# Kernel tuning notes

Hardware: AMD Instinct MI355X
Metric: run time of the kernel (lower is better)

## Reference

```python
import jax, jax.numpy as jnp
import numpy as np

N_NODES = 50000
N_EDGES = 800000
FEAT_DIM = 64


def setup_inputs() -> dict:
    key = jax.random.key(0)
    k1, k2, k3 = jax.random.split(key, 3)
    x = jax.random.normal(k1, (N_NODES, FEAT_DIM), dtype=jnp.float32)
    beta = jnp.ones((1,), dtype=jnp.float32)
    # CSR-equivalent edge list: sorted destination rows + random source columns
    row_index = jnp.sort(jax.random.randint(k2, (N_EDGES,), 0, N_NODES, dtype=jnp.int32))
    col_index = jax.random.randint(k3, (N_EDGES,), 0, N_NODES, dtype=jnp.int32)
    return {"x": x, "beta": beta, "row_index": row_index, "col_index": col_index}


def reference(x, beta, row_index, col_index):
    """AGNN layer: SDDMM edge attention (beta * cosine similarity) over the
    sparse graph, per-row softmax, then sparse neighbor aggregation.
    Equivalent math to mygraph.SDDMM + mygraph.agnn_udf (select_id == 5).
    x: [N, D]; row_index/col_index: [E] edge endpoints (row = destination).
    """
    N = x.shape[0]
    eps = 1e-8
    # L2-normalize node features for cosine similarity
    xn = x * jax.lax.rsqrt(jnp.sum(x * x, axis=-1, keepdims=True) + eps)  # [N, D]
    # SDDMM: attention only on existing edges
    att = beta[0] * jnp.sum(xn[row_index] * xn[col_index], axis=-1)  # [E]
    # Numerically stable segment softmax over each destination row
    m = jax.ops.segment_max(att, row_index, num_segments=N)  # [N]
    m = jnp.where(jnp.isfinite(m), m, 0.0)  # empty rows -> -inf guard
    e = jnp.exp(att - m[row_index])  # [E]
    denom = jax.ops.segment_sum(e, row_index, num_segments=N)  # [N]
    alpha = e / jnp.maximum(denom[row_index], 1e-16)  # [E]
    # Sparse aggregation: out_i = sum_j alpha_ij * x_j
    out = jax.ops.segment_sum(alpha[:, None] * x[col_index], row_index, num_segments=N)
    return out
```

## Files before the change

### kernel.cpp

```cpp
#include <hip/hip_runtime.h>
#include <hip/hip_bf16.h>

#define FEAT 64

__global__ void prep_kernel(const float* __restrict__ x,
                            float* __restrict__ rn,
                            const int* __restrict__ row,
                            int* __restrict__ row_ptr,
                            int N, int E, int normBlocks) {
    if ((int)blockIdx.x < normBlocks) {
        int wid  = blockIdx.x * (blockDim.x >> 6) + (threadIdx.x >> 6);
        int lane = threadIdx.x & 63;
        int g    = lane >> 3;
        int sub  = lane & 7;
        int r    = wid * 8 + g;
        if (r >= N) return;
        const char* xB = (const char*)x;
        uint roff = ((uint)r << 8) + ((uint)sub << 4);
        float4 xa = *reinterpret_cast<const float4*>(xB + roff);
        float4 xb = *reinterpret_cast<const float4*>(xB + roff + 128);
        float q = xa.x*xa.x + xa.y*xa.y + xa.z*xa.z + xa.w*xa.w
                + xb.x*xb.x + xb.y*xb.y + xb.z*xb.z + xb.w*xb.w;
        q += __shfl_xor(q, 1);
        q += __shfl_xor(q, 2);
        q += __shfl_xor(q, 4);
        if (sub == 0) rn[r] = rsqrtf(q + 1e-8f);
    } else {
        int e = (blockIdx.x - normBlocks) * blockDim.x + threadIdx.x;
        if (e >= E) return;
        int curr = row[e];
        if (e == 0) {
            for (int r = 0; r <= curr; ++r) row_ptr[r] = 0;
        } else {
            int prev = row[e - 1];
            for (int r = prev + 1; r <= curr; ++r) row_ptr[r] = e;
        }
        if (e == E - 1) {
            for (int r = curr + 1; r <= N; ++r) row_ptr[r] = E;
        }
    }
}

__global__ void fused_kernel(const float* __restrict__ x,
                             const float* __restrict__ rn,
                             const float* __restrict__ beta,
                             const int* __restrict__ row_ptr,
                             const int* __restrict__ col,
                             float* __restrict__ out, int N) {
    int wid  = blockIdx.x * (blockDim.x >> 6) + (threadIdx.x >> 6);
    int lane = threadIdx.x & 63;
    int slot = lane >> 4;
    int h    = (lane >> 3) & 1;
    int sub  = lane & 7;
    int r    = wid * 4 + slot;
    bool rv  = (r < N);

    int start = 0, deg = 0;
    if (rv) {
        start = row_ptr[r];
        deg   = row_ptr[r + 1] - start;
    }

    const char* xB   = (const char*)x;
    uint        subo = (uint)sub << 4;

    int   colsA = 0, colsB = 0;
    float rnsA  = 0.f, rnsB = 0.f;
    if (sub < deg)     { colsA = col[start + sub];     rnsA = rn[colsA]; }
    if (8 + sub < deg) { colsB = col[start + 8 + sub]; rnsB = rn[colsB]; }

    float4 xa = make_float4(0.f, 0.f, 0.f, 0.f);
    float4 xb = make_float4(0.f, 0.f, 0.f, 0.f);
    if (rv) {
        uint roff = ((uint)r << 8) + subo;
        xa = *reinterpret_cast<const float4*>(xB + roff);
        xb = *reinterpret_cast<const float4*>(xB + roff + 128);
        float brn = beta[0] * rn[r];
        xa.x *= brn; xa.y *= brn; xa.z *= brn; xa.w *= brn;
        xb.x *= brn; xb.y *= brn; xb.z *= brn; xb.w *= brn;
    }

    float  s = 0.f;
    float4 aa = make_float4(0.f, 0.f, 0.f, 0.f);
    float4 ab = make_float4(0.f, 0.f, 0.f, 0.f);

    for (int base = 0; base < deg; base += 4) {
        if (base && (base & 7) == 0) {
            colsA = colsB;  rnsA = rnsB;
            if (base + 8 + sub < deg) {
                colsB = col[start + base + 8 + sub];
                rnsB  = rn[colsB];
            }
        }
        int  k0 = base + 2 * h;
        int  kk = (base & 7) + 2 * h;
        bool v0 = k0 < deg;
        bool v1 = k0 + 1 < deg;

        int   c0  = __shfl(colsA, kk, 8);
        float rn0 = __shfl(rnsA,  kk, 8);
        int   c1  = __shfl(colsA, kk + 1, 8);
        float rn1 = __shfl(rnsA,  kk + 1, 8);

        float4 va0 = make_float4(0.f, 0.f, 0.f, 0.f);
        float4 vb0 = make_float4(0.f, 0.f, 0.f, 0.f);
        float4 va1 = make_float4(0.f, 0.f, 0.f, 0.f);
        float4 vb1 = make_float4(0.f, 0.f, 0.f, 0.f);
        if (v0) {
            uint o0 = ((uint)c0 << 8) + subo;
            va0 = *reinterpret_cast<const float4*>(xB + o0);
            vb0 = *reinterpret_cast<const float4*>(xB + o0 + 128);
        }
        if (v1) {
            uint o1 = ((uint)c1 << 8) + subo;
            va1 = *reinterpret_cast<const float4*>(xB + o1);
            vb1 = *reinterpret_cast<const float4*>(xB + o1 + 128);
        }

        float d0 = xa.x*va0.x + xa.y*va0.y + xa.z*va0.z + xa.w*va0.w
                 + xb.x*vb0.x + xb.y*vb0.y + xb.z*vb0.z + xb.w*vb0.w;
        float d1 = xa.x*va1.x + xa.y*va1.y + xa.z*va1.z + xa.w*va1.w
                 + xb.x*vb1.x + xb.y*vb1.y + xb.z*vb1.z + xb.w*vb1.w;
        d0 += __shfl_xor(d0, 1);  d1 += __shfl_xor(d1, 1);
        d0 += __shfl_xor(d0, 2);  d1 += __shfl_xor(d1, 2);
        d0 += __shfl_xor(d0, 4);  d1 += __shfl_xor(d1, 4);

        float e0 = v0 ? __expf(d0 * rn0) : 0.f;
        float e1 = v1 ? __expf(d1 * rn1) : 0.f;
        s += e0 + e1;

        aa.x += e0 * va0.x + e1 * va1.x;  aa.y += e0 * va0.y + e1 * va1.y;
        aa.z += e0 * va0.z + e1 * va1.z;  aa.w += e0 * va0.w + e1 * va1.w;
        ab.x += e0 * vb0.x + e1 * vb1.x;  ab.y += e0 * vb0.y + e1 * vb1.y;
        ab.z += e0 * vb0.z + e1 * vb1.z;  ab.w += e0 * vb0.w + e1 * vb1.w;
    }

    s    += __shfl_xor(s, 8);
    aa.x += __shfl_xor(aa.x, 8);  aa.y += __shfl_xor(aa.y, 8);
    aa.z += __shfl_xor(aa.z, 8);  aa.w += __shfl_xor(aa.w, 8);
    ab.x += __shfl_xor(ab.x, 8);  ab.y += __shfl_xor(ab.y, 8);
    ab.z += __shfl_xor(ab.z, 8);  ab.w += __shfl_xor(ab.w, 8);

    float inv = 1.0f / fmaxf(s, 1e-16f);
    if (rv) {
        float4 o = h ? ab : aa;
        uint roff = ((uint)r << 8) + subo + ((uint)h << 7);
        *reinterpret_cast<float4*>((char*)out + roff) =
            make_float4(o.x * inv, o.y * inv, o.z * inv, o.w * inv);
    }
}

extern "C" void kernel_launch(void* const* d_in, const int* in_sizes, int n_in,
                              void* d_out, int out_size, void* d_ws, size_t ws_size,
                              hipStream_t stream) {
    const float* x    = (const float*)d_in[0];
    const float* beta = (const float*)d_in[1];
    const int*   row  = (const int*)d_in[2];
    const int*   col  = (const int*)d_in[3];
    float*       out  = (float*)d_out;

    const int N = in_sizes[0] / FEAT;
    const int E = in_sizes[2];

    float* rn      = (float*)d_ws;
    int*   row_ptr = (int*)(rn + ((N + 63) & ~63));

    {
        int normBlocks = (N + 31) / 32;
        int edgeBlocks = (E + 255) / 256;
        prep_kernel<<<normBlocks + edgeBlocks, 256, 0, stream>>>(
            x, rn, row, row_ptr, N, E, normBlocks);
    }
    {
        int waves = (N + 3) / 4;
        int grid  = (waves + 3) / 4;
        fused_kernel<<<grid, 256, 0, stream>>>(x, rn, beta, row_ptr, col, out, N);
    }
}
```

Before: 40.03 us.

## Gather neighbor features from a bf16 copy with software-pipelined prefetch

The prep kernel now also writes a bf16-packed copy of x (128 bytes per row) into the workspace. A new fused kernel gathers neighbor rows from that copy, which halves gather bytes. It processes 8 rows per wave with 4 edges per iteration and prefetches the next group's packed rows before computing the current one. Neighbor features used in both the attention dot product and the aggregation are rounded to bf16, which adds accuracy risk, and the path only runs when the workspace is large enough.

New measurement: 38.29 us. -4.3%, faster.

```diff
diff --git a/kernel.cpp b/kernel.cpp
--- a/kernel.cpp
+++ b/kernel.cpp
@@ -3,8 +3,27 @@
 
 #define FEAT 64
 
+__device__ inline uint packbf2(float lo, float hi) {
+    uint ul = __float_as_uint(lo), uh = __float_as_uint(hi);
+    ul += 0x7FFFu + ((ul >> 16) & 1u);
+    uh += 0x7FFFu + ((uh >> 16) & 1u);
+    return (ul >> 16) | (uh & 0xFFFF0000u);
+}
+
+__device__ inline void unpack8(uint4 q, float4& va, float4& vb) {
+    va.x = __uint_as_float(q.x << 16);
+    va.y = __uint_as_float(q.x & 0xFFFF0000u);
+    va.z = __uint_as_float(q.y << 16);
+    va.w = __uint_as_float(q.y & 0xFFFF0000u);
+    vb.x = __uint_as_float(q.z << 16);
+    vb.y = __uint_as_float(q.z & 0xFFFF0000u);
+    vb.z = __uint_as_float(q.w << 16);
+    vb.w = __uint_as_float(q.w & 0xFFFF0000u);
+}
+
 __global__ void prep_kernel(const float* __restrict__ x,
                             float* __restrict__ rn,
+                            uint4* __restrict__ xh,
                             const int* __restrict__ row,
                             int* __restrict__ row_ptr,
                             int N, int E, int normBlocks) {
@@ -25,6 +44,14 @@
         q += __shfl_xor(q, 2);
         q += __shfl_xor(q, 4);
         if (sub == 0) rn[r] = rsqrtf(q + 1e-8f);
+        if (xh) {
+            uint4 p;
+            p.x = packbf2(xa.x, xa.y);
+            p.y = packbf2(xa.z, xa.w);
+            p.z = packbf2(xb.x, xb.y);
+            p.w = packbf2(xb.z, xb.w);
+            xh[r * 8 + sub] = p;
+        }
     } else {
         int e = (blockIdx.x - normBlocks) * blockDim.x + threadIdx.x;
         if (e >= E) return;
@@ -38,6 +65,133 @@
         if (e == E - 1) {
             for (int r = curr + 1; r <= N; ++r) row_ptr[r] = E;
         }
+    }
+}
+
+__global__ void fused_bf16_kernel(const float* __restrict__ x,
+                                  const uint4* __restrict__ xh,
+                                  const float* __restrict__ rn,
+                                  const float* __restrict__ beta,
+                                  const int* __restrict__ row_ptr,
+                                  const int* __restrict__ col,
+                                  float* __restrict__ out, int N) {
+    int wid  = blockIdx.x * (blockDim.x >> 6) + (threadIdx.x >> 6);
+    int lane = threadIdx.x & 63;
+    int g    = lane >> 3;
+    int sub  = lane & 7;
+    int r    = wid * 8 + g;
+    bool rv  = (r < N);
+
+    int start = 0, deg = 0;
+    if (rv) {
+        start = row_ptr[r];
+        deg   = row_ptr[r + 1] - start;
+    }
+
+    int   colsA = 0, colsB = 0;
+    float rnsA  = 0.f, rnsB = 0.f;
+    if (sub < deg)     { colsA = col[start + sub];     rnsA = rn[colsA]; }
+    if (8 + sub < deg) { colsB = col[start + 8 + sub]; rnsB = rn[colsB]; }
+
+    float4 xa = make_float4(0.f, 0.f, 0.f, 0.f);
+    float4 xb = make_float4(0.f, 0.f, 0.f, 0.f);
+    if (rv) {
+        const char* xB = (const char*)x;
+        uint roff = ((uint)r << 8) + ((uint)sub << 4);
+        xa = *reinterpret_cast<const float4*>(xB + roff);
+        xb = *reinterpret_cast<const float4*>(xB + roff + 128);
+        float brn = beta[0] * rn[r];
+        xa.x *= brn; xa.y *= brn; xa.z *= brn; xa.w *= brn;
+        xb.x *= brn; xb.y *= brn; xb.z *= brn; xb.w *= brn;
+    }
+
+    float  s = 0.f;
+    float4 aa = make_float4(0.f, 0.f, 0.f, 0.f);
+    float4 ab = make_float4(0.f, 0.f, 0.f, 0.f);
+
+    uint4 z4 = make_uint4(0u, 0u, 0u, 0u);
+    uint4 q0 = z4, q1 = z4, q2 = z4, q3 = z4;
+    float rn0 = 0.f, rn1 = 0.f, rn2 = 0.f, rn3 = 0.f;
+
+    {
+        int   c0 = __shfl(colsA, 0, 8), c1 = __shfl(colsA, 1, 8);
+        int   c2 = __shfl(colsA, 2, 8), c3 = __shfl(colsA, 3, 8);
+        rn0 = __shfl(rnsA, 0, 8);  rn1 = __shfl(rnsA, 1, 8);
+        rn2 = __shfl(rnsA, 2, 8);  rn3 = __shfl(rnsA, 3, 8);
+        if (0 < deg) q0 = xh[c0 * 8 + sub];
+        if (1 < deg) q1 = xh[c1 * 8 + sub];
+        if (2 < deg) q2 = xh[c2 * 8 + sub];
+        if (3 < deg) q3 = xh[c3 * 8 + sub];
+    }
+
+    for (int base = 0; base < deg; base += 4) {
+        if (base && (base & 7) == 0) {
+            colsA = colsB;  rnsA = rnsB;
+            colsB = 0;      rnsB = 0.f;
+            if (base + 8 + sub < deg) {
+                colsB = col[start + base + 8 + sub];
+                rnsB  = rn[colsB];
+            }
+        }
+        int  nb  = base + 4;
+        int  nkk = nb & 7;
+        int   cS = (nkk == 4) ? colsA : colsB;
+        float rS = (nkk == 4) ? rnsA  : rnsB;
+        int   nc0 = __shfl(cS, nkk + 0, 8), nc1 = __shfl(cS, nkk + 1, 8);
+        int   nc2 = __shfl(cS, nkk + 2, 8), nc3 = __shfl(cS, nkk + 3, 8);
+        float nr0 = __shfl(rS, nkk + 0, 8), nr1 = __shfl(rS, nkk + 1, 8);
+        float nr2 = __shfl(rS, nkk + 2, 8), nr3 = __shfl(rS, nkk + 3, 8);
+        uint4 nq0 = z4, nq1 = z4, nq2 = z4, nq3 = z4;
+        if (nb + 0 < deg) nq0 = xh[nc0 * 8 + sub];
+        if (nb + 1 < deg) nq1 = xh[nc1 * 8 + sub];
+        if (nb + 2 < deg) nq2 = xh[nc2 * 8 + sub];
+        if (nb + 3 < deg) nq3 = xh[nc3 * 8 + sub];
+
+        float4 va0, vb0, va1, vb1, va2, vb2, va3, vb3;
+        unpack8(q0, va0, vb0);  unpack8(q1, va1, vb1);
+        unpack8(q2, va2, vb2);  unpack8(q3, va3, vb3);
+
+        float d0 = xa.x*va0.x + xa.y*va0.y + xa.z*va0.z + xa.w*va0.w
+                 + xb.x*vb0.x + xb.y*vb0.y + xb.z*vb0.z + xb.w*vb0.w;
+        float d1 = xa.x*va1.x + xa.y*va1.y + xa.z*va1.z + xa.w*va1.w
+                 + xb.x*vb1.x + xb.y*vb1.y + xb.z*vb1.z + xb.w*vb1.w;
+        float d2 = xa.x*va2.x + xa.y*va2.y + xa.z*va2.z + xa.w*va2.w
+                 + xb.x*vb2.x + xb.y*vb2.y + xb.z*vb2.z + xb.w*vb2.w;
+        float d3 = xa.x*va3.x + xa.y*va3.y + xa.z*va3.z + xa.w*va3.w
+                 + xb.x*vb3.x + xb.y*vb3.y + xb.z*vb3.z + xb.w*vb3.w;
+        d0 += __shfl_xor(d0, 1);  d1 += __shfl_xor(d1, 1);
+        d2 += __shfl_xor(d2, 1);  d3 += __shfl_xor(d3, 1);
+        d0 += __shfl_xor(d0, 2);  d1 += __shfl_xor(d1, 2);
+        d2 += __shfl_xor(d2, 2);  d3 += __shfl_xor(d3, 2);
+        d0 += __shfl_xor(d0, 4);  d1 += __shfl_xor(d1, 4);
+        d2 += __shfl_xor(d2, 4);  d3 += __shfl_xor(d3, 4);
+
+        float e0 = (base + 0 < deg) ? __expf(d0 * rn0) : 0.f;
+        float e1 = (base + 1 < deg) ? __expf(d1 * rn1) : 0.f;
+        float e2 = (base + 2 < deg) ? __expf(d2 * rn2) : 0.f;
+        float e3 = (base + 3 < deg) ? __expf(d3 * rn3) : 0.f;
+        s += (e0 + e1) + (e2 + e3);
+
+        aa.x += e0*va0.x + e1*va1.x + e2*va2.x + e3*va3.x;
+        aa.y += e0*va0.y + e1*va1.y + e2*va2.y + e3*va3.y;
+        aa.z += e0*va0.z + e1*va1.z + e2*va2.z + e3*va3.z;
+        aa.w += e0*va0.w + e1*va1.w + e2*va2.w + e3*va3.w;
+        ab.x += e0*vb0.x + e1*vb1.x + e2*vb2.x + e3*vb3.x;
+        ab.y += e0*vb0.y + e1*vb1.y + e2*vb2.y + e3*vb3.y;
+        ab.z += e0*vb0.z + e1*vb1.z + e2*vb2.z + e3*vb3.z;
+        ab.w += e0*vb0.w + e1*vb1.w + e2*vb2.w + e3*vb3.w;
+
+        q0 = nq0; q1 = nq1; q2 = nq2; q3 = nq3;
+        rn0 = nr0; rn1 = nr1; rn2 = nr2; rn3 = nr3;
+    }
+
+    float inv = 1.0f / fmaxf(s, 1e-16f);
+    if (rv) {
+        uint roff = ((uint)r << 8) + ((uint)sub << 4);
+        *reinterpret_cast<float4*>((char*)out + roff) =
+            make_float4(aa.x * inv, aa.y * inv, aa.z * inv, aa.w * inv);
+        *reinterpret_cast<float4*>((char*)out + roff + 128) =
+            make_float4(ab.x * inv, ab.y * inv, ab.z * inv, ab.w * inv);
     }
 }
 
@@ -98,9 +252,9 @@
         bool v1 = k0 + 1 < deg;
 
         int   c0  = __shfl(colsA, kk, 8);
-        float rn0 = __shfl(rnsA,  kk, 8);
+        float rw0 = __shfl(rnsA,  kk, 8);
         int   c1  = __shfl(colsA, kk + 1, 8);
-        float rn1 = __shfl(rnsA,  kk + 1, 8);
+        float rw1 = __shfl(rnsA,  kk + 1, 8);
 
         float4 va0 = make_float4(0.f, 0.f, 0.f, 0.f);
         float4 vb0 = make_float4(0.f, 0.f, 0.f, 0.f);
@@ -125,8 +279,8 @@
         d0 += __shfl_xor(d0, 2);  d1 += __shfl_xor(d1, 2);
         d0 += __shfl_xor(d0, 4);  d1 += __shfl_xor(d1, 4);
 
-        float e0 = v0 ? __expf(d0 * rn0) : 0.f;
-        float e1 = v1 ? __expf(d1 * rn1) : 0.f;
+        float e0 = v0 ? __expf(d0 * rw0) : 0.f;
+        float e1 = v1 ? __expf(d1 * rw1) : 0.f;
         s += e0 + e1;
 
         aa.x += e0 * va0.x + e1 * va1.x;  aa.y += e0 * va0.y + e1 * va1.y;
@@ -162,18 +316,30 @@
     const int N = in_sizes[0] / FEAT;
     const int E = in_sizes[2];
 
-    float* rn      = (float*)d_ws;
-    int*   row_ptr = (int*)(rn + ((N + 63) & ~63));
+    char*  ws      = (char*)d_ws;
+    size_t off_rp  = ((size_t)(N + 64) * 4 + 511) & ~(size_t)511;
+    size_t off_xh  = off_rp + (((size_t)(N + 1) * 4 + 511) & ~(size_t)511);
+    size_t need    = off_xh + (size_t)N * 128;
+
+    float* rn      = (float*)ws;
+    int*   row_ptr = (int*)(ws + off_rp);
+    uint4* xh      = (ws_size >= need) ? (uint4*)(ws + off_xh) : nullptr;
 
     {
         int normBlocks = (N + 31) / 32;
         int edgeBlocks = (E + 255) / 256;
         prep_kernel<<<normBlocks + edgeBlocks, 256, 0, stream>>>(
-            x, rn, row, row_ptr, N, E, normBlocks);
-    }
-    {
+            x, rn, xh, row, row_ptr, N, E, normBlocks);
+    }
+    if (xh) {
+        int waves = (N + 7) / 8;
+        int grid  = (waves + 3) / 4;
+        fused_bf16_kernel<<<grid, 256, 0, stream>>>(
+            x, xh, rn, beta, row_ptr, col, out, N);
+    } else {
         int waves = (N + 3) / 4;
         int grid  = (waves + 3) / 4;
-        fused_kernel<<<grid, 256, 0, stream>>>(x, rn, beta, row_ptr, col, out, N);
-    }
-}
+        fused_kernel<<<grid, 256, 0, stream>>>(
+            x, rn, beta, row_ptr, col, out, N);
+    }
+}
```
